# Kernel tuning notes

Measured on AMD Instinct MI355X. Metric: run time of the kernel, lower is better.

Reference implementation:

```python
import jax, jax.numpy as jnp
import numpy as np

UNITS = 256


def setup_inputs() -> dict:
    key = jax.random.key(0)
    ks = jax.random.split(key, 9)
    B, H, W, C = 8, 64, 64, UNITS
    x = jax.random.normal(ks[0], (B, H, W, C), dtype=jnp.float32)
    # 1x1 Conv2D == per-pixel linear: weight [C_in, C_out], bias [C_out]
    def lin(k):
        return jax.random.normal(k, (C, UNITS), dtype=jnp.float32) * (2.0 / C) ** 0.5
    return {
        "x": x,
        "wq": lin(ks[1]), "bq": jnp.zeros((UNITS,), jnp.float32),
        "wk": lin(ks[2]), "bk": jnp.zeros((UNITS,), jnp.float32),
        "wv": lin(ks[3]), "bv": jnp.zeros((UNITS,), jnp.float32),
        "wp": lin(ks[4]), "bp": jnp.zeros((UNITS,), jnp.float32),
    }


def reference(x, wq, bq, wk, bk, wv, bv, wp, bp):
    B, H, W, C = x.shape
    N = H * W
    scale = jnp.asarray(UNITS, jnp.float32) ** -0.5
    xf = x.reshape(B, N, C)  # 1x1 conv == matmul over channels
    q = xf @ wq + bq
    k = xf @ wk + bk
    v = xf @ wv + bv
    # (b,h,w,c)x(b,H,W,c)->(b,h,w,H,W) flattened to (b,N,N)
    scores = jnp.einsum('bnc,bmc->bnm', q, k) * scale
    attn = jax.nn.softmax(scores, axis=-1)
    out = jnp.einsum('bnm,bmc->bnc', attn, v)
    proj = out @ wp + bp
    return x + proj.reshape(B, H, W, UNITS)
```

## Files before the change

### kernel.cpp

```cpp
#include <hip/hip_runtime.h>


typedef _Float16 half8 __attribute__((ext_vector_type(8)));
typedef float f32x4 __attribute__((ext_vector_type(4)));
typedef unsigned int u32x4 __attribute__((ext_vector_type(4)));
typedef unsigned int u32x2 __attribute__((ext_vector_type(2)));

#define MFMA16(a, b, c) __builtin_amdgcn_mfma_f32_16x16x32_f16((a), (b), (c), 0, 0, 0)

#if __has_builtin(__builtin_amdgcn_exp2f)
#define EXP2(x) __builtin_amdgcn_exp2f(x)
#else
#define EXP2(x) exp2f(x)
#endif

#define QSCALE 0.09016843898f
#define ESHIFT 11.5415603f

__device__ __forceinline__ void lds_load16(const _Float16* g, _Float16* l) {
    __builtin_amdgcn_global_load_lds(
        (const __attribute__((address_space(1))) unsigned int*)g,
        (__attribute__((address_space(3))) unsigned int*)l, 16, 0, 0);
}

__global__ __launch_bounds__(256)
void wt_prep(const float* __restrict__ w0, const float* __restrict__ w1,
             const float* __restrict__ w2, const float* __restrict__ w3,
             _Float16* __restrict__ outw)
{
    __shared__ _Float16 sT[64 * 72];
    const int z = blockIdx.z;
    const float* W = (z == 0) ? w0 : (z == 1) ? w1 : (z == 2) ? w2 : w3;
    _Float16* O = outw + z * 65536;
    const int kb = blockIdx.x * 64, nb = blockIdx.y * 64;
    const int t = threadIdx.x;
    const int r = t >> 4, c4 = (t & 15) * 4;
#pragma unroll
    for (int i = 0; i < 4; ++i) {
        f32x4 ld = *(const f32x4*)(W + (size_t)(kb + r + i * 16) * 256 + nb + c4);
#pragma unroll
        for (int j = 0; j < 4; ++j) sT[(c4 + j) * 72 + r + i * 16] = (_Float16)ld[j];
    }
    __syncthreads();
#pragma unroll
    for (int i = 0; i < 4; ++i) {
        int n = r + i * 16;
        *(u32x2*)&O[(size_t)(nb + n) * 256 + kb + c4] = *(const u32x2*)&sT[n * 72 + c4];
    }
}

__global__ __launch_bounds__(256)
void qkv_gemm(const float* __restrict__ x, const _Float16* __restrict__ wt,
              const float* __restrict__ bq, const float* __restrict__ bk,
              const float* __restrict__ bv,
              _Float16* __restrict__ qo, _Float16* __restrict__ ko,
              _Float16* __restrict__ vo)
{
    __shared__ _Float16 smem[4 * 2560];
    _Float16* sA = smem;

    const int tid  = threadIdx.x;
    const int w    = tid >> 6;
    const int lane = tid & 63;
    const int quad = lane >> 4;
    const int l16  = lane & 15;
    const int m0   = blockIdx.x * 64;
    const int n0   = blockIdx.y * 64;
    const int rS = tid >> 2, cS = (tid & 3) << 3;

    const float* ap = x + (size_t)(m0 + rS) * 256 + cS;
    f32x4 a0 = *(const f32x4*)ap, a1 = *(const f32x4*)(ap + 4);
    u32x4 bst[3];
#pragma unroll
    for (int o = 0; o < 3; ++o)
        bst[o] = *(const u32x4*)(wt + o * 65536 + (size_t)(n0 + rS) * 256 + cS);

    f32x4 zero4 = {0.f, 0.f, 0.f, 0.f};
    f32x4 acc[3][4];
#pragma unroll
    for (int o = 0; o < 3; ++o)
#pragma unroll
        for (int nt = 0; nt < 4; ++nt) acc[o][nt] = zero4;

    for (int it = 0; it < 8; ++it) {
        __syncthreads();
        half8 t;
#pragma unroll
        for (int j = 0; j < 4; ++j) { t[j] = (_Float16)a0[j]; t[j + 4] = (_Float16)a1[j]; }
        *(half8*)&sA[rS * 40 + cS] = t;
#pragma unroll
        for (int o = 0; o < 3; ++o)
            *(u32x4*)&smem[2560 * (o + 1) + rS * 40 + cS] = bst[o];
        __syncthreads();
        if (it < 7) {
            int k0 = (it + 1) * 32;
            const float* ap2 = x + (size_t)(m0 + rS) * 256 + k0 + cS;
            a0 = *(const f32x4*)ap2; a1 = *(const f32x4*)(ap2 + 4);
#pragma unroll
            for (int o = 0; o < 3; ++o)
                bst[o] = *(const u32x4*)(wt + o * 65536 + (size_t)(n0 + rS) * 256 + k0 + cS);
        }
        half8 af = *(const half8*)&sA[(16 * w + l16) * 40 + quad * 8];
#pragma unroll
        for (int o = 0; o < 3; ++o)
#pragma unroll
            for (int nt = 0; nt < 4; ++nt) {
                half8 bf = *(const half8*)&smem[2560 * (o + 1) + (nt * 16 + l16) * 40 + quad * 8];
                acc[o][nt] = MFMA16(af, bf, acc[o][nt]);
            }
    }

#pragma unroll
    for (int nt = 0; nt < 4; ++nt) {
#pragma unroll
        for (int reg = 0; reg < 4; ++reg) {
            int row = m0 + 16 * w + quad * 4 + reg;
            int col = n0 + nt * 16 + l16;
            qo[(size_t)row * 256 + col] = (_Float16)((acc[0][nt][reg] + bq[col]) * QSCALE);
            ko[(size_t)row * 256 + col] = (_Float16)(acc[1][nt][reg] + bk[col]);
        }
    }
    __syncthreads();
    _Float16* sT = smem;
#pragma unroll
    for (int nt = 0; nt < 4; ++nt)
#pragma unroll
        for (int reg = 0; reg < 4; ++reg)
            sT[(nt * 16 + l16) * 72 + 16 * w + quad * 4 + reg] =
                (_Float16)(acc[2][nt][reg] + bv[n0 + nt * 16 + l16]);
    __syncthreads();
    int ch = tid >> 2, po = (tid & 3) << 4;
    int bb = m0 >> 12, pix = m0 & 4095;
    _Float16* dst = vo + (size_t)bb * 1048576 + (size_t)(n0 + ch) * 4096 + pix + po;
    *(u32x4*)dst       = *(const u32x4*)&sT[ch * 72 + po];
    *(u32x4*)(dst + 8) = *(const u32x4*)&sT[ch * 72 + po + 8];
}

__global__ __launch_bounds__(256)
void proj_gemm(const _Float16* __restrict__ opart, const float* __restrict__ lpart,
               const _Float16* __restrict__ Wt, const float* __restrict__ bias,
               const float* __restrict__ resid, float* __restrict__ out)
{
    __shared__ _Float16 smem[2 * 2560];
    _Float16* sA = smem;
    _Float16* sB = smem + 2560;

    const int tid  = threadIdx.x;
    const int w    = tid >> 6;
    const int lane = tid & 63;
    const int quad = lane >> 4;
    const int l16  = lane & 15;
    const int m0   = blockIdx.x * 64;
    const int n0   = blockIdx.y * 64;
    const int rS = tid >> 2, cS = (tid & 3) << 3;

    const _Float16* o1p = opart;
    const _Float16* o2p = opart + 8388608;
    const int row = m0 + rS;
    const float inv = 1.0f / (lpart[row] + lpart[32768 + row]);

    u32x4 a1v = *(const u32x4*)(o1p + (size_t)row * 256 + cS);
    u32x4 a2v = *(const u32x4*)(o2p + (size_t)row * 256 + cS);
    u32x4 bst = *(const u32x4*)(Wt + (size_t)(n0 + rS) * 256 + cS);

    f32x4 zero4 = {0.f, 0.f, 0.f, 0.f};
    f32x4 acc[4] = {zero4, zero4, zero4, zero4};

    for (int it = 0; it < 8; ++it) {
        __syncthreads();
        {
            half8 h1 = *(half8*)&a1v, h2 = *(half8*)&a2v, t;
#pragma unroll
            for (int j = 0; j < 8; ++j)
                t[j] = (_Float16)(((float)h1[j] + (float)h2[j]) * inv);
            *(half8*)&sA[rS * 40 + cS] = t;
        }
        *(u32x4*)&sB[rS * 40 + cS] = bst;
        __syncthreads();
        if (it < 7) {
            int k0 = (it + 1) * 32;
            a1v = *(const u32x4*)(o1p + (size_t)row * 256 + k0 + cS);
            a2v = *(const u32x4*)(o2p + (size_t)row * 256 + k0 + cS);
            bst = *(const u32x4*)(Wt + (size_t)(n0 + rS) * 256 + k0 + cS);
        }
        half8 af = *(const half8*)&sA[(16 * w + l16) * 40 + quad * 8];
#pragma unroll
        for (int nt = 0; nt < 4; ++nt) {
            half8 bf = *(const half8*)&sB[(nt * 16 + l16) * 40 + quad * 8];
            acc[nt] = MFMA16(af, bf, acc[nt]);
        }
    }
#pragma unroll
    for (int nt = 0; nt < 4; ++nt) {
#pragma unroll
        for (int reg = 0; reg < 4; ++reg) {
            int orow = m0 + 16 * w + quad * 4 + reg;
            int col = n0 + nt * 16 + l16;
            out[(size_t)orow * 256 + col] =
                acc[nt][reg] + bias[col] + resid[(size_t)orow * 256 + col];
        }
    }
}

__global__ __launch_bounds__(256, 2)
void attn_kernel(const _Float16* __restrict__ q, const _Float16* __restrict__ k,
                 const _Float16* __restrict__ vt, _Float16* __restrict__ opart,
                 float* __restrict__ lpart)
{
    extern __shared__ _Float16 smem[];
    _Float16* sKb = smem;
    _Float16* sVb = smem + 16384;

    const int tid  = threadIdx.x;
    const int w    = tid >> 6;
    const int lane = tid & 63;
    const int quad = lane >> 4;
    const int l16  = lane & 15;
    const int x7   = l16 & 7;
    const int kh   = blockIdx.x & 1;
    const int qt   = (blockIdx.x >> 1) & 31;
    const int b    = blockIdx.x >> 6;

    _Float16* sPw = smem + 32768 + w * 1280;

    const _Float16* kb = k  + (size_t)b * 1048576 + (size_t)kh * 524288;
    const _Float16* vb = vt + (size_t)b * 1048576 + kh * 2048;
    const int rowbase = qt * 128 + w * 32;

    half8 qf0[8], qf1[8];
    {
        const _Float16* q0 = q + (size_t)(b * 4096 + rowbase + l16) * 256 + quad * 8;
        const _Float16* q1 = q0 + 16 * 256;
#pragma unroll
        for (int kk = 0; kk < 8; ++kk) {
            qf0[kk] = *(const half8*)(q0 + kk * 32);
            qf1[kk] = *(const half8*)(q1 + kk * 32);
        }
    }

    f32x4 zero4 = {0.f, 0.f, 0.f, 0.f};
    f32x4 o0[16], o1[16];
#pragma unroll
    for (int i = 0; i < 16; ++i) { o0[i] = zero4; o1[i] = zero4; }
    float ls0[4] = {0.f, 0.f, 0.f, 0.f}, ls1[4] = {0.f, 0.f, 0.f, 0.f};

    const int hi = lane >> 5, lo31 = lane & 31;
    const int chS = (lane >> 2);
    const int cvS = (lane & 3) ^ (lane >> 4);

#pragma unroll
    for (int j = 0; j < 4; ++j) {
        int cc = w * 4 + j;
        int r = cc * 2 + hi;
        int c = lo31 ^ (r & 7);
        lds_load16(kb + (size_t)r * 256 + c * 8, sKb + cc * 512);
        int ch = cc * 16 + chS;
        lds_load16(vb + (size_t)ch * 4096 + cvS * 8, sVb + cc * 512);
    }

    for (int kt = 0; kt < 64; ++kt) {
        const int p = kt & 1;
        __syncthreads();

        if (kt < 63) {
            const _Float16* ktb = kb + (size_t)(kt + 1) * 8192;
            const _Float16* vtb = vb + (kt + 1) * 32;
            _Float16* dK = sKb + (1 - p) * 8192;
            _Float16* dV = sVb + (1 - p) * 8192;
#pragma unroll
            for (int j = 0; j < 4; ++j) {
                int cc = w * 4 + j;
                int r = cc * 2 + hi;
                int c = lo31 ^ (r & 7);
                lds_load16(ktb + (size_t)r * 256 + c * 8, dK + cc * 512);
                int ch = cc * 16 + chS;
                lds_load16(vtb + (size_t)ch * 4096 + cvS * 8, dV + cc * 512);
            }
        }

        const _Float16* K = sKb + p * 8192;
        const _Float16* V = sVb + p * 8192;

        f32x4 s0[2] = {zero4, zero4};
        f32x4 s1[2] = {zero4, zero4};
#pragma unroll
        for (int kk = 0; kk < 8; ++kk) {
            const int cb = ((kk * 4 + quad) ^ x7) * 8;
#pragma unroll
            for (int nt = 0; nt < 2; ++nt) {
                half8 bf = *(const half8*)&K[(nt * 16 + l16) * 256 + cb];
                s0[nt] = MFMA16(qf0[kk], bf, s0[nt]);
                s1[nt] = MFMA16(qf1[kk], bf, s1[nt]);
            }
        }

#pragma unroll
        for (int reg = 0; reg < 4; ++reg) {
            float p0 = EXP2(s0[0][reg] - ESHIFT);
            float p1 = EXP2(s0[1][reg] - ESHIFT);
            ls0[reg] += p0 + p1;
            int pr = (quad * 4 + reg) * 40 + l16;
            sPw[pr]      = (_Float16)p0;
            sPw[pr + 16] = (_Float16)p1;
            float p2 = EXP2(s1[0][reg] - ESHIFT);
            float p3 = EXP2(s1[1][reg] - ESHIFT);
            ls1[reg] += p2 + p3;
            int pr1 = (16 + quad * 4 + reg) * 40 + l16;
            sPw[pr1]      = (_Float16)p2;
            sPw[pr1 + 16] = (_Float16)p3;
        }
        __asm__ volatile("s_waitcnt lgkmcnt(0)" ::: "memory");
        half8 pf0 = *(const half8*)&sPw[l16 * 40 + quad * 8];
        half8 pf1 = *(const half8*)&sPw[(16 + l16) * 40 + quad * 8];

        const int cv = (quad ^ ((l16 >> 2) & 3)) * 8;
#pragma unroll
        for (int nt = 0; nt < 16; ++nt) {
            half8 bf = *(const half8*)&V[(nt * 16 + l16) * 32 + cv];
            o0[nt] = MFMA16(pf0, bf, o0[nt]);
            o1[nt] = MFMA16(pf1, bf, o1[nt]);
        }
    }

#pragma unroll
    for (int reg = 0; reg < 4; ++reg) {
#pragma unroll
        for (int d = 1; d < 16; d <<= 1) {
            ls0[reg] += __shfl_xor(ls0[reg], d);
            ls1[reg] += __shfl_xor(ls1[reg], d);
        }
    }
    _Float16* po = opart + (size_t)kh * 8388608 + (size_t)(b * 4096 + rowbase) * 256;
    float* pl = lpart + kh * 32768 + b * 4096 + rowbase;
#pragma unroll
    for (int reg = 0; reg < 4; ++reg) {
        int r0 = quad * 4 + reg;
        int r1 = r0 + 16;
#pragma unroll
        for (int nt = 0; nt < 16; ++nt) {
            po[(size_t)r0 * 256 + nt * 16 + l16] = (_Float16)o0[nt][reg];
            po[(size_t)r1 * 256 + nt * 16 + l16] = (_Float16)o1[nt][reg];
        }
        if (l16 == 0) { pl[r0] = ls0[reg]; pl[r1] = ls1[reg]; }
    }
}

extern "C" void kernel_launch(void* const* d_in, const int* in_sizes, int n_in,
                              void* d_out, int out_size, void* d_ws, size_t ws_size,
                              hipStream_t stream) {
    const float* x  = (const float*)d_in[0];
    const float* wq = (const float*)d_in[1];
    const float* bq = (const float*)d_in[2];
    const float* wk = (const float*)d_in[3];
    const float* bk = (const float*)d_in[4];
    const float* wv = (const float*)d_in[5];
    const float* bv = (const float*)d_in[6];
    const float* wp = (const float*)d_in[7];
    const float* bp = (const float*)d_in[8];

    _Float16* qws  = (_Float16*)d_ws;
    _Float16* kws  = qws + 8388608;
    _Float16* vtws = kws + 8388608;
    _Float16* ows  = vtws + 8388608;
    _Float16* wt   = ows + 16777216;
    float*    lws  = (float*)(wt + 262144);

    dim3 blk(256);

    (void)hipFuncSetAttribute((const void*)attn_kernel,
                              hipFuncAttributeMaxDynamicSharedMemorySize, 75776);

    wt_prep<<<dim3(4, 4, 4), blk, 0, stream>>>(wq, wk, wv, wp, wt);
    qkv_gemm<<<dim3(512, 4), blk, 0, stream>>>(x, wt, bq, bk, bv, qws, kws, vtws);
    attn_kernel<<<dim3(512), blk, 75776, stream>>>(qws, kws, vtws, ows, lws);
    proj_gemm<<<dim3(512, 4), blk, 0, stream>>>(ows, lws, wt + 196608, bp, x, (float*)d_out);
}
```

Baseline: 319.7 us.

## Switch attention kernel to 32x32x16 MFMA with transposed score tile and fragment-native LDS layout

Rewrites the attention inner loop to use 32x32x16 MFMA instructions instead of 16x16x32. The score tile is computed as K·Qᵀ so each lane holds one query row's probabilities, and the row-sum becomes a single cross-half shuffle. K and V tiles are staged in LDS in the per-lane fragment order, so each MFMA operand is a contiguous lane-indexed 16-byte read and the XOR swizzling is gone. This is meant to cut LDS reads per FLOP and instruction overhead, at the cost of a new P staging layout and different output store patterns.

```diff
diff --git a/kernel.cpp b/kernel.cpp
--- a/kernel.cpp
+++ b/kernel.cpp
@@ -2,11 +2,14 @@
 
 
 typedef _Float16 half8 __attribute__((ext_vector_type(8)));
+typedef _Float16 half4 __attribute__((ext_vector_type(4)));
 typedef float f32x4 __attribute__((ext_vector_type(4)));
+typedef float f32x16 __attribute__((ext_vector_type(16)));
 typedef unsigned int u32x4 __attribute__((ext_vector_type(4)));
 typedef unsigned int u32x2 __attribute__((ext_vector_type(2)));
 
 #define MFMA16(a, b, c) __builtin_amdgcn_mfma_f32_16x16x32_f16((a), (b), (c), 0, 0, 0)
+#define MFMA32(a, b, c) __builtin_amdgcn_mfma_f32_32x32x16_f16((a), (b), (c), 0, 0, 0)
 
 #if __has_builtin(__builtin_amdgcn_exp2f)
 #define EXP2(x) __builtin_amdgcn_exp2f(x)
@@ -17,7 +20,7 @@
 #define QSCALE 0.09016843898f
 #define ESHIFT 11.5415603f
 
-__device__ __forceinline__ void lds_load16(const _Float16* g, _Float16* l) {
+__device__ __forceinline__ void lds_load16(const void* g, void* l) {
     __builtin_amdgcn_global_load_lds(
         (const __attribute__((address_space(1))) unsigned int*)g,
         (__attribute__((address_space(3))) unsigned int*)l, 16, 0, 0);
@@ -207,55 +210,48 @@
                  const _Float16* __restrict__ vt, _Float16* __restrict__ opart,
                  float* __restrict__ lpart)
 {
-    extern __shared__ _Float16 smem[];
-    _Float16* sKb = smem;
-    _Float16* sVb = smem + 16384;
+    extern __shared__ char smem[];
+    char* sKb = smem;
+    char* sVb = smem + 32768;
 
     const int tid  = threadIdx.x;
     const int w    = tid >> 6;
     const int lane = tid & 63;
-    const int quad = lane >> 4;
-    const int l16  = lane & 15;
-    const int x7   = l16 & 7;
+    const int l31  = lane & 31;
+    const int hi   = lane >> 5;
     const int kh   = blockIdx.x & 1;
     const int qt   = (blockIdx.x >> 1) & 31;
     const int b    = blockIdx.x >> 6;
 
-    _Float16* sPw = smem + 32768 + w * 1280;
+    char* sPw = smem + 65536 + w * 2560;
 
     const _Float16* kb = k  + (size_t)b * 1048576 + (size_t)kh * 524288;
     const _Float16* vb = vt + (size_t)b * 1048576 + kh * 2048;
     const int rowbase = qt * 128 + w * 32;
 
-    half8 qf0[8], qf1[8];
+    half8 qf[16];
     {
-        const _Float16* q0 = q + (size_t)(b * 4096 + rowbase + l16) * 256 + quad * 8;
-        const _Float16* q1 = q0 + 16 * 256;
-#pragma unroll
-        for (int kk = 0; kk < 8; ++kk) {
-            qf0[kk] = *(const half8*)(q0 + kk * 32);
-            qf1[kk] = *(const half8*)(q1 + kk * 32);
-        }
-    }
-
-    f32x4 zero4 = {0.f, 0.f, 0.f, 0.f};
-    f32x4 o0[16], o1[16];
-#pragma unroll
-    for (int i = 0; i < 16; ++i) { o0[i] = zero4; o1[i] = zero4; }
-    float ls0[4] = {0.f, 0.f, 0.f, 0.f}, ls1[4] = {0.f, 0.f, 0.f, 0.f};
-
-    const int hi = lane >> 5, lo31 = lane & 31;
-    const int chS = (lane >> 2);
-    const int cvS = (lane & 3) ^ (lane >> 4);
+        const _Float16* q0 = q + (size_t)(b * 4096 + rowbase + l31) * 256 + hi * 8;
+#pragma unroll
+        for (int s = 0; s < 16; ++s) qf[s] = *(const half8*)(q0 + s * 16);
+    }
+
+    f32x16 o[8];
+#pragma unroll
+    for (int i = 0; i < 8; ++i)
+#pragma unroll
+        for (int j = 0; j < 16; ++j) o[i][j] = 0.f;
+    float ls = 0.f;
+
+    const int koffL = l31 * 256 + hi * 8;
 
 #pragma unroll
     for (int j = 0; j < 4; ++j) {
-        int cc = w * 4 + j;
-        int r = cc * 2 + hi;
-        int c = lo31 ^ (r & 7);
-        lds_load16(kb + (size_t)r * 256 + c * 8, sKb + cc * 512);
-        int ch = cc * 16 + chS;
-        lds_load16(vb + (size_t)ch * 4096 + cvS * 8, sVb + cc * 512);
+        int s = w * 4 + j;
+        lds_load16(kb + koffL + s * 16, sKb + s * 1024);
+        int ct = s >> 1, ks = s & 1;
+        lds_load16(vb + (size_t)(32 * ct + l31) * 4096 + 16 * ks + 8 * hi,
+                   sVb + s * 1024);
     }
 
     for (int kt = 0; kt < 64; ++kt) {
@@ -265,83 +261,66 @@
         if (kt < 63) {
             const _Float16* ktb = kb + (size_t)(kt + 1) * 8192;
             const _Float16* vtb = vb + (kt + 1) * 32;
-            _Float16* dK = sKb + (1 - p) * 8192;
-            _Float16* dV = sVb + (1 - p) * 8192;
+            char* dK = sKb + (1 - p) * 16384;
+            char* dV = sVb + (1 - p) * 16384;
 #pragma unroll
             for (int j = 0; j < 4; ++j) {
-                int cc = w * 4 + j;
-                int r = cc * 2 + hi;
-                int c = lo31 ^ (r & 7);
-                lds_load16(ktb + (size_t)r * 256 + c * 8, dK + cc * 512);
-                int ch = cc * 16 + chS;
-                lds_load16(vtb + (size_t)ch * 4096 + cvS * 8, dV + cc * 512);
+                int s = w * 4 + j;
+                lds_load16(ktb + koffL + s * 16, dK + s * 1024);
+                int ct = s >> 1, ks = s & 1;
+                lds_load16(vtb + (size_t)(32 * ct + l31) * 4096 + 16 * ks + 8 * hi,
+                           dV + s * 1024);
             }
         }
 
-        const _Float16* K = sKb + p * 8192;
-        const _Float16* V = sVb + p * 8192;
-
-        f32x4 s0[2] = {zero4, zero4};
-        f32x4 s1[2] = {zero4, zero4};
-#pragma unroll
-        for (int kk = 0; kk < 8; ++kk) {
-            const int cb = ((kk * 4 + quad) ^ x7) * 8;
-#pragma unroll
-            for (int nt = 0; nt < 2; ++nt) {
-                half8 bf = *(const half8*)&K[(nt * 16 + l16) * 256 + cb];
-                s0[nt] = MFMA16(qf0[kk], bf, s0[nt]);
-                s1[nt] = MFMA16(qf1[kk], bf, s1[nt]);
-            }
-        }
-
-#pragma unroll
-        for (int reg = 0; reg < 4; ++reg) {
-            float p0 = EXP2(s0[0][reg] - ESHIFT);
-            float p1 = EXP2(s0[1][reg] - ESHIFT);
-            ls0[reg] += p0 + p1;
-            int pr = (quad * 4 + reg) * 40 + l16;
-            sPw[pr]      = (_Float16)p0;
-            sPw[pr + 16] = (_Float16)p1;
-            float p2 = EXP2(s1[0][reg] - ESHIFT);
-            float p3 = EXP2(s1[1][reg] - ESHIFT);
-            ls1[reg] += p2 + p3;
-            int pr1 = (16 + quad * 4 + reg) * 40 + l16;
-            sPw[pr1]      = (_Float16)p2;
-            sPw[pr1 + 16] = (_Float16)p3;
+        const char* K = sKb + p * 16384;
+        const char* V = sVb + p * 16384;
+
+        f32x16 sacc;
+#pragma unroll
+        for (int j = 0; j < 16; ++j) sacc[j] = 0.f;
+#pragma unroll
+        for (int s = 0; s < 16; ++s) {
+            half8 af = *(const half8*)(K + s * 1024 + lane * 16);
+            sacc = MFMA32(af, qf[s], sacc);
+        }
+
+#pragma unroll
+        for (int rb = 0; rb < 4; ++rb) {
+            float p0 = EXP2(sacc[rb * 4 + 0] - ESHIFT);
+            float p1 = EXP2(sacc[rb * 4 + 1] - ESHIFT);
+            float p2 = EXP2(sacc[rb * 4 + 2] - ESHIFT);
+            float p3 = EXP2(sacc[rb * 4 + 3] - ESHIFT);
+            ls += (p0 + p1) + (p2 + p3);
+            half4 t;
+            t[0] = (_Float16)p0; t[1] = (_Float16)p1;
+            t[2] = (_Float16)p2; t[3] = (_Float16)p3;
+            *(half4*)(sPw + l31 * 80 + (8 * rb + 4 * hi) * 2) = t;
         }
         __asm__ volatile("s_waitcnt lgkmcnt(0)" ::: "memory");
-        half8 pf0 = *(const half8*)&sPw[l16 * 40 + quad * 8];
-        half8 pf1 = *(const half8*)&sPw[(16 + l16) * 40 + quad * 8];
-
-        const int cv = (quad ^ ((l16 >> 2) & 3)) * 8;
-#pragma unroll
-        for (int nt = 0; nt < 16; ++nt) {
-            half8 bf = *(const half8*)&V[(nt * 16 + l16) * 32 + cv];
-            o0[nt] = MFMA16(pf0, bf, o0[nt]);
-            o1[nt] = MFMA16(pf1, bf, o1[nt]);
-        }
-    }
-
-#pragma unroll
-    for (int reg = 0; reg < 4; ++reg) {
-#pragma unroll
-        for (int d = 1; d < 16; d <<= 1) {
-            ls0[reg] += __shfl_xor(ls0[reg], d);
-            ls1[reg] += __shfl_xor(ls1[reg], d);
-        }
-    }
+        half8 pf0 = *(const half8*)(sPw + l31 * 80 + hi * 16);
+        half8 pf1 = *(const half8*)(sPw + l31 * 80 + 32 + hi * 16);
+
+#pragma unroll
+        for (int ct = 0; ct < 8; ++ct) {
+            half8 b0 = *(const half8*)(V + (ct * 2 + 0) * 1024 + lane * 16);
+            half8 b1 = *(const half8*)(V + (ct * 2 + 1) * 1024 + lane * 16);
+            o[ct] = MFMA32(pf0, b0, o[ct]);
+            o[ct] = MFMA32(pf1, b1, o[ct]);
+        }
+    }
+
+    ls += __shfl_xor(ls, 32);
     _Float16* po = opart + (size_t)kh * 8388608 + (size_t)(b * 4096 + rowbase) * 256;
     float* pl = lpart + kh * 32768 + b * 4096 + rowbase;
-#pragma unroll
-    for (int reg = 0; reg < 4; ++reg) {
-        int r0 = quad * 4 + reg;
-        int r1 = r0 + 16;
-#pragma unroll
-        for (int nt = 0; nt < 16; ++nt) {
-            po[(size_t)r0 * 256 + nt * 16 + l16] = (_Float16)o0[nt][reg];
-            po[(size_t)r1 * 256 + nt * 16 + l16] = (_Float16)o1[nt][reg];
-        }
-        if (l16 == 0) { pl[r0] = ls0[reg]; pl[r1] = ls1[reg]; }
+    if (hi == 0) pl[l31] = ls;
+#pragma unroll
+    for (int ct = 0; ct < 8; ++ct) {
+#pragma unroll
+        for (int reg = 0; reg < 16; ++reg) {
+            int row = (reg & 3) + 8 * (reg >> 2) + 4 * hi;
+            po[(size_t)row * 256 + ct * 32 + l31] = (_Float16)o[ct][reg];
+        }
     }
 }
 
```

New measurement: 316.4 us. About the same (-1.0%).
